# Optimization experiments

Hardware: AMD Instinct MI355X
Metric: run time of the kernel (lower is better)

## Reference

```python
import jax, jax.numpy as jnp
import numpy as np

IMAGE_TOKEN_INDEX = -200
B, N, D = 2, 768, 2048          # batch, seq, llm_size
CLIP = 1024                      # clip hidden size
NUM_HEADS = 8
HEAD_DIM = CLIP // NUM_HEADS
NUM_LAYER, LAYER_RATE = 24, 4
LAYER_IDX = np.asarray(NUM_LAYER - np.arange(0, NUM_LAYER + 1, LAYER_RATE))  # [24,20,16,12,8,4,0]
J = len(LAYER_IDX)               # 7 selected layers
L = NUM_LAYER + 1                # 25 stacked layers in all_features
IMG, PATCH = 336, 14
HP = IMG // PATCH                # 24 patches per side; patch_ratio == 1
HW = HP * HP                     # 576 vision tokens
SL = HP * (HP + 1) + 1           # 601 = H*(W+1)+1 ragged slice length
SCALE = CLIP ** (-0.5)
LN_EPS = 1e-5
COS_EPS = 1e-8


def setup_inputs() -> dict:
    key = jax.random.key(0)
    ks = jax.random.split(key, 10)
    input_ids = jax.random.randint(ks[0], (B, N), 0, 32000)
    pos = jnp.array([37, 111])  # image-token positions; pos + SL <= N
    input_ids = input_ids.at[jnp.arange(B), pos].set(IMAGE_TOKEN_INDEX)
    rgb = jax.random.normal(ks[1], (B, 3, IMG, IMG), dtype=jnp.float32)
    mask = jnp.ones((B, 1, IMG, IMG), dtype=jnp.float32)  # last channel: all-ones mask
    images = jnp.concatenate([rgb, mask], axis=1)
    all_features = jax.random.normal(ks[2], (B, N, L, D), dtype=jnp.float32)
    patch_hw = jnp.full((B, 2), HP, dtype=jnp.int32)
    s = 0.02
    return {
        'input_ids': input_ids,
        'images': images,
        'all_features': all_features,
        'patch_hw': patch_hw,
        'norm_gamma': jnp.ones((J, D), dtype=jnp.float32),
        'norm_beta': jnp.zeros((J, D), dtype=jnp.float32),
        'norm_w': jax.random.normal(ks[3], (J, CLIP, D), dtype=jnp.float32) * s,
        'input_w': jax.random.normal(ks[4], (CLIP, D), dtype=jnp.float32) * s,
        'input_b': jnp.zeros((CLIP,), dtype=jnp.float32),
        'output_w': jax.random.normal(ks[5], (CLIP, CLIP), dtype=jnp.float32) * s,
        'output_b': jnp.zeros((CLIP,), dtype=jnp.float32),
        'clip_w': jax.random.normal(ks[6], (CLIP, 3 * PATCH * PATCH), dtype=jnp.float32) * s,
        'clip_b': jnp.zeros((CLIP,), dtype=jnp.float32),
    }


def reference(input_ids, images, all_features, patch_hw,
              norm_gamma, norm_beta, norm_w,
              input_w, input_b, output_w, output_b, clip_w, clip_b):
    # clip_layer modeled as a frozen 14x14 patch-embed linear -> [B, HW, CLIP]
    patches = images[:, :3].reshape(B, 3, HP, PATCH, HP, PATCH)
    patches = patches.transpose(0, 2, 4, 1, 3, 5).reshape(B, HW, 3 * PATCH * PATCH)
    clip_feats = patches @ clip_w.T + clip_b  # [B, HW, CLIP]
    # mask channel is all ones -> pooled clip_2d_mask keeps every patch
    lidx = jnp.asarray(LAYER_IDX)

    def per_sample(ids, feats, cf):
        # ragged slice at the image token (data-dependent start, fixed length)
        idx = jnp.argmax(ids == IMAGE_TOKEN_INDEX)
        f = jax.lax.dynamic_slice_in_dim(feats, idx, SL, axis=0)[1:]      # [600, L, D]
        # [L,D,H,W+1] drop-last-col in torch == row-major split here
        f = f.reshape(HP, HP + 1, L, D)[:, :HP].reshape(HW, L, D)          # [576, L, D]
        # per-layer LayerNorm + no-bias Linear on 7 selected layers
        xj = f[:, lidx]                                                    # [HW, J, D]
        mu = xj.mean(-1, keepdims=True)
        var = ((xj - mu) ** 2).mean(-1, keepdims=True)
        xn = (xj - mu) / jnp.sqrt(var + LN_EPS) * norm_gamma + norm_beta
        vis = jnp.einsum('njd,jcd->njc', xn, norm_w)                       # [HW, J, CLIP]
        inp = f[:, -1] @ input_w.T + input_b                               # [HW, CLIP]
        # single-query multi-head cross attention over the J-1 kv layers
        q = vis[:, 0].reshape(HW, NUM_HEADS, HEAD_DIM)                     # [HW, h, d]
        kv = vis[:, 1:].reshape(HW, J - 1, NUM_HEADS, HEAD_DIM).transpose(0, 2, 1, 3)  # [HW, h, J-1, d]
        attn = jax.nn.softmax((q[:, :, None, :] * SCALE * kv).sum(-1), axis=-1)        # [HW, h, J-1]
        fuse = (attn[..., None] * kv).sum(-2).reshape(HW, CLIP)
        out = inp + fuse @ output_w.T + output_b                           # [HW, CLIP]
        denom = jnp.maximum(jnp.linalg.norm(out, axis=-1) * jnp.linalg.norm(cf, axis=-1), COS_EPS)
        cos = (out * cf).sum(-1) / denom
        return 1.0 - cos.mean()

    losses = jax.vmap(per_sample)(input_ids, all_features, clip_feats)
    return losses.mean()  # mse_loss / count_image with count_image == B
```

## Files before the change

kernel.cpp:

```cpp
#include <hip/hip_runtime.h>

#define HW_   576
#define BHW   1152
#define DD    2048
#define CLIPC 1024
#define NSEQ  768
#define LL    25
#define KPAD  640

#define ASCALE 8.0f
#define BSCALE 32.0f
#define INV_AB (1.0f/256.0f)

typedef __bf16 bf16x8 __attribute__((ext_vector_type(8)));
typedef float  f32x4  __attribute__((ext_vector_type(4)));
typedef int    i32x8  __attribute__((ext_vector_type(8)));
typedef unsigned short u16;
typedef unsigned char  u8;

__device__ __forceinline__ float bf2f(u16 u){
  union { unsigned int i; float f; } v; v.i = ((unsigned int)u) << 16; return v.f;
}
__device__ __forceinline__ u16 f2bf(float f){
  union { float f; unsigned int i; } v; v.f = f;
  unsigned int u = v.i;
  return (u16)((u + 0x7fffu + ((u >> 16) & 1u)) >> 16);
}
__device__ __forceinline__ unsigned int pk2bf(float a, float b){
  return ((unsigned int)f2bf(a)) | (((unsigned int)f2bf(b)) << 16);
}
__device__ __forceinline__ unsigned int pk4_fp8(float a, float b, float c, float d){
  int v = 0;
  v = __builtin_amdgcn_cvt_pk_fp8_f32(a, b, v, false);
  v = __builtin_amdgcn_cvt_pk_fp8_f32(c, d, v, true);
  return (unsigned int)v;
}

__device__ __forceinline__ void gld_lds16(const void* g, void* l){
  __builtin_amdgcn_global_load_lds((__attribute__((address_space(1))) void*)g,
                                   (__attribute__((address_space(3))) void*)l,
                                   16, 0, 0);
}

__global__ void setup_k(const int* __restrict__ ids, int* __restrict__ idxbuf,
                        float* __restrict__ rowacc){
  const int lane = threadIdx.x;
  for (int b = 0; b < 2; b++){
    int best = 0x7fffffff;
    for (int i = lane; i < NSEQ; i += 64)
      if (ids[b*NSEQ + i] == -200 && i < best) best = i;
    for (int off = 32; off; off >>= 1){ int o = __shfl_xor(best, off); best = min(best, o); }
    if (lane == 0) idxbuf[b] = best;
  }
  for (int i = lane; i < BHW*4; i += 64) rowacc[i] = 0.f;
}

__global__ void prep_k(const float* __restrict__ norm_w, const float* __restrict__ input_w,
                       const float* __restrict__ output_w, const float* __restrict__ clip_w,
                       const float* __restrict__ images, const float* __restrict__ feats,
                       const int* __restrict__ idxbuf,
                       const float* __restrict__ gamma, const float* __restrict__ beta,
                       u8* __restrict__ B8, u16* __restrict__ inpw, u16* __restrict__ outw,
                       u16* __restrict__ clipw, u16* __restrict__ patch,
                       u8* __restrict__ A8, u16* __restrict__ A7){
  const int blk = blockIdx.x, tid = threadIdx.x;
  if (blk < 7168){
    long idx = (long)blk*2048 + tid*8;
    float4 v0 = *(const float4*)(norm_w + idx);
    float4 v1 = *(const float4*)(norm_w + idx + 4);
    uint2 o;
    o.x = pk4_fp8(v0.x*BSCALE, v0.y*BSCALE, v0.z*BSCALE, v0.w*BSCALE);
    o.y = pk4_fp8(v1.x*BSCALE, v1.y*BSCALE, v1.z*BSCALE, v1.w*BSCALE);
    *(uint2*)(B8 + idx) = o;
    return;
  }
  if (blk < 8704){
    const bool isInp = (blk < 8192);
    long idx = (long)(blk - (isInp ? 7168 : 8192))*2048 + tid*8;
    const float* s = isInp ? (input_w + idx) : (output_w + idx);
    float4 v0 = *(const float4*)s;
    float4 v1 = *(const float4*)(s + 4);
    uint4 o = { pk2bf(v0.x,v0.y), pk2bf(v0.z,v0.w), pk2bf(v1.x,v1.y), pk2bf(v1.z,v1.w) };
    *(uint4*)((isInp ? inpw : outw) + idx) = o;
    return;
  }
  if (blk < 9728){
    const int c = blk - 8704;
    for (int k = tid; k < KPAD; k += 256)
      clipw[c*KPAD + k] = (k < 588) ? f2bf(clip_w[c*588 + k]) : (u16)0;
    return;
  }
  if (blk < 10880){
    const int r = blk - 9728;
    const int b = r / HW_, n = r % HW_;
    const int hi = n / 24, wi = n % 24;
    for (int p = tid; p < KPAD; p += 256){
      float v = 0.f;
      if (p < 588){
        int c3 = p / 196, rem = p - c3*196;
        int ph = rem / 14, pw = rem - ph*14;
        v = images[(((long)b*4 + c3)*336 + hi*14 + ph)*336 + wi*14 + pw];
      }
      patch[(long)r*KPAD + p] = f2bf(v);
    }
    return;
  }
  const int q = blk - 10880;
  const int r = q >> 3, g = q & 7;
  const int b = r / HW_, n = r % HW_;
  const int hi = n / 24, wi = n % 24;
  const int tok = idxbuf[b] + 1 + hi*25 + wi;
  const int layer = (g < 7) ? (24 - g*4) : 24;
  const float* src = feats + (((long)(b*NSEQ + tok))*LL + layer)*DD + tid*8;
  float4 a = *(const float4*)src;
  float4 c = *(const float4*)(src + 4);
  if (g == 7){
    uint4 o = { pk2bf(a.x,a.y), pk2bf(a.z,a.w), pk2bf(c.x,c.y), pk2bf(c.z,c.w) };
    *(uint4*)(A7 + (long)r*DD + tid*8) = o;
    return;
  }
  float s  = a.x+a.y+a.z+a.w + c.x+c.y+c.z+c.w;
  float qq = a.x*a.x+a.y*a.y+a.z*a.z+a.w*a.w + c.x*c.x+c.y*c.y+c.z*c.z+c.w*c.w;
  for (int off = 32; off; off >>= 1){ s += __shfl_xor(s, off); qq += __shfl_xor(qq, off); }
  __shared__ float rs[4], rq[4];
  const int wave = tid >> 6, lane = tid & 63;
  if (lane == 0){ rs[wave] = s; rq[wave] = qq; }
  __syncthreads();
  const float ts = rs[0]+rs[1]+rs[2]+rs[3];
  const float tq = rq[0]+rq[1]+rq[2]+rq[3];
  const float mu   = ts * (1.f/2048.f);
  const float var  = tq * (1.f/2048.f) - mu*mu;
  const float rstd = rsqrtf(var + 1e-5f);
  const float4 g0 = *(const float4*)(gamma + g*DD + tid*8);
  const float4 g1 = *(const float4*)(gamma + g*DD + tid*8 + 4);
  const float4 b0 = *(const float4*)(beta  + g*DD + tid*8);
  const float4 b1 = *(const float4*)(beta  + g*DD + tid*8 + 4);
  uint2 o;
  o.x = pk4_fp8(((a.x-mu)*rstd*g0.x + b0.x)*ASCALE, ((a.y-mu)*rstd*g0.y + b0.y)*ASCALE,
                ((a.z-mu)*rstd*g0.z + b0.z)*ASCALE, ((a.w-mu)*rstd*g0.w + b0.w)*ASCALE);
  o.y = pk4_fp8(((c.x-mu)*rstd*g1.x + b1.x)*ASCALE, ((c.y-mu)*rstd*g1.y + b1.y)*ASCALE,
                ((c.z-mu)*rstd*g1.z + b1.z)*ASCALE, ((c.w-mu)*rstd*g1.w + b1.w)*ASCALE);
  *(uint2*)(A8 + ((long)g*BHW + r)*DD + tid*8) = o;
}

__global__ __launch_bounds__(256, 3)
void gemm_fp8_k(const u8* __restrict__ A_all, const u8* __restrict__ B_all,
                u16* __restrict__ C_all){
  __shared__ alignas(16) u8 As[128*128];
  __shared__ alignas(16) u8 Bs[128*128];
  const int z = blockIdx.z;
  const u8* Az = A_all + (long)z*BHW*DD;
  const u8* Bz = B_all + (long)z*CLIPC*DD;
  const int bm = blockIdx.x*128, bn = blockIdx.y*128;
  const int tid = threadIdx.x, wave = tid >> 6, lane = tid & 63;
  const int l15 = lane & 15, quad = lane >> 4;
  const int wr = (wave >> 1)*64, wc = (wave & 1)*64;
  f32x4 acc[4][4] = {};

  const int laneRow   = lane >> 3;
  const int laneChunk = (lane & 7) ^ laneRow;
  const u8* gA = Az + (long)(bm + wave*32 + laneRow)*DD + laneChunk*16;
  const u8* gB = Bz + (long)(bn + wave*32 + laneRow)*DD + laneChunk*16;
  u8* lA = &As[wave*32*128];
  u8* lB = &Bs[wave*32*128];
  const long rs8 = 8L*DD;

  for (int k0 = 0; k0 < DD; k0 += 128){
#pragma unroll
    for (int t = 0; t < 4; t++) gld_lds16(gA + k0 + t*rs8, lA + t*1024);
#pragma unroll
    for (int t = 0; t < 4; t++) gld_lds16(gB + k0 + t*rs8, lB + t*1024);
    __syncthreads();
    i32x8 af[4], bg[4];
    const int sw = l15 & 7;
#pragma unroll
    for (int i = 0; i < 4; i++){
      const u8* rp = &As[(wr + i*16 + l15)*128];
      uint4 lo = *(const uint4*)(rp + (((quad*2 + 0) ^ sw)*16));
      uint4 hi = *(const uint4*)(rp + (((quad*2 + 1) ^ sw)*16));
      af[i] = (i32x8){(int)lo.x,(int)lo.y,(int)lo.z,(int)lo.w,
                      (int)hi.x,(int)hi.y,(int)hi.z,(int)hi.w};
    }
#pragma unroll
    for (int j = 0; j < 4; j++){
      const u8* rp = &Bs[(wc + j*16 + l15)*128];
      uint4 lo = *(const uint4*)(rp + (((quad*2 + 0) ^ sw)*16));
      uint4 hi = *(const uint4*)(rp + (((quad*2 + 1) ^ sw)*16));
      bg[j] = (i32x8){(int)lo.x,(int)lo.y,(int)lo.z,(int)lo.w,
                      (int)hi.x,(int)hi.y,(int)hi.z,(int)hi.w};
    }
#pragma unroll
    for (int i = 0; i < 4; i++)
#pragma unroll
      for (int j = 0; j < 4; j++)
        acc[i][j] = __builtin_amdgcn_mfma_scale_f32_16x16x128_f8f6f4(
            af[i], bg[j], acc[i][j], 0, 0, 0, 0x7F7F7F7F, 0, 0x7F7F7F7F);
    __syncthreads();
  }

  u16* C = C_all + (long)z*BHW*CLIPC;
#pragma unroll
  for (int i = 0; i < 4; i++)
#pragma unroll
    for (int j = 0; j < 4; j++)
#pragma unroll
      for (int rr = 0; rr < 4; rr++){
        const int row = bm + wr + i*16 + quad*4 + rr;
        const int col = bn + wc + j*16 + l15;
        C[(long)row*CLIPC + col] = f2bf(acc[i][j][rr] * INV_AB);
      }
}

__device__ __forceinline__ void gemm_core(const u16* __restrict__ Az, const u16* __restrict__ Bz,
                                          int K, int bm, int bn,
                                          u16* __restrict__ As, u16* __restrict__ Bs,
                                          f32x4 (&acc)[4][4]){
  const int tid  = threadIdx.x;
  const int wave = tid >> 6, lane = tid & 63;
  const int l15 = lane & 15, quad = lane >> 4;
  const int wr = (wave >> 1) * 64, wc = (wave & 1) * 64;
  const int laneRow = lane >> 3;
  const int laneCol = (((lane & 7) ^ laneRow) * 8);
  const u16* gA = Az + (long)(bm + wave*32 + laneRow)*K + laneCol;
  const u16* gB = Bz + (long)(bn + wave*32 + laneRow)*K + laneCol;
  u16* lA = &As[wave*2048];
  u16* lB = &Bs[wave*2048];
  const long rs8 = (long)8 * K;

  for (int k0 = 0; k0 < K; k0 += 64){
#pragma unroll
    for (int t = 0; t < 4; t++) gld_lds16(gA + k0 + t*rs8, lA + t*512);
#pragma unroll
    for (int t = 0; t < 4; t++) gld_lds16(gB + k0 + t*rs8, lB + t*512);
    __syncthreads();
#pragma unroll
    for (int s = 0; s < 2; s++){
      bf16x8 af[4], bg[4];
#pragma unroll
      for (int i = 0; i < 4; i++)
        af[i] = *(const bf16x8*)&As[(wr + i*16 + l15)*64 + (((s*4 + quad) ^ (l15 & 7)) * 8)];
#pragma unroll
      for (int j = 0; j < 4; j++)
        bg[j] = *(const bf16x8*)&Bs[(wc + j*16 + l15)*64 + (((s*4 + quad) ^ (l15 & 7)) * 8)];
#pragma unroll
      for (int i = 0; i < 4; i++)
#pragma unroll
        for (int j = 0; j < 4; j++)
          acc[i][j] = __builtin_amdgcn_mfma_f32_16x16x32_bf16(af[i], bg[j], acc[i][j], 0, 0, 0);
    }
    __syncthreads();
  }
}

__global__ __launch_bounds__(256, 3)
void gemm_misc_k(const u16* __restrict__ patch, const u16* __restrict__ clipw,
                 const u16* __restrict__ A7, const u16* __restrict__ inpw,
                 float* __restrict__ cf, u16* __restrict__ C7,
                 const float* __restrict__ clip_b, const float* __restrict__ input_b){
  __shared__ alignas(16) u16 As[128*64];
  __shared__ alignas(16) u16 Bs[128*64];
  const int z = blockIdx.z;
  const int bm = blockIdx.x*128, bn = blockIdx.y*128;
  const u16* Az = z ? A7 : patch;
  const u16* Bz = z ? inpw : clipw;
  const int K = z ? DD : KPAD;
  f32x4 acc[4][4] = {};
  gemm_core(Az, Bz, K, bm, bn, As, Bs, acc);

  const int lane = threadIdx.x & 63, wave = threadIdx.x >> 6;
  const int l15 = lane & 15, quad = lane >> 4;
  const int wr = (wave >> 1)*64, wc = (wave & 1)*64;
#pragma unroll
  for (int i = 0; i < 4; i++)
#pragma unroll
    for (int j = 0; j < 4; j++)
#pragma unroll
      for (int rr = 0; rr < 4; rr++){
        const int row = bm + wr + i*16 + quad*4 + rr;
        const int col = bn + wc + j*16 + l15;
        if (z) C7[(long)row*CLIPC + col] = f2bf(acc[i][j][rr] + input_b[col]);
        else   cf[(long)row*CLIPC + col] = acc[i][j][rr] + clip_b[col];
      }
}

__global__ void attn_k(const u16* __restrict__ C_all, u16* __restrict__ fuse){
  const int r = blockIdx.x;
  const int h = (blockIdx.y << 2) | (threadIdx.x >> 6);
  const int lane = threadIdx.x & 63;
  const long slot = (long)BHW * CLIPC;
  const long rb = (long)r * CLIPC;
  const int c0 = h*128 + lane, c1 = c0 + 64;
  const float q0 = bf2f(C_all[rb + c0]), q1 = bf2f(C_all[rb + c1]);
  float k0v[6], k1v[6], dt[6];
#pragma unroll
  for (int t = 0; t < 6; t++){
    const u16* base = C_all + (long)(t+1)*slot + rb;
    k0v[t] = bf2f(base[c0]); k1v[t] = bf2f(base[c1]);
    dt[t] = q0*k0v[t] + q1*k1v[t];
  }
#pragma unroll
  for (int t = 0; t < 6; t++)
    for (int off = 32; off; off >>= 1) dt[t] += __shfl_xor(dt[t], off);
  float l[6], e[6];
#pragma unroll
  for (int t = 0; t < 6; t++) l[t] = dt[t] * 0.03125f;
  float m = l[0];
#pragma unroll
  for (int t = 1; t < 6; t++) m = fmaxf(m, l[t]);
  float ssum = 0.f;
#pragma unroll
  for (int t = 0; t < 6; t++){ e[t] = __expf(l[t] - m); ssum += e[t]; }
  const float inv = 1.f / ssum;
  float f0 = 0.f, f1 = 0.f;
#pragma unroll
  for (int t = 0; t < 6; t++){ const float a = e[t]*inv; f0 += a*k0v[t]; f1 += a*k1v[t]; }
  fuse[rb + c0] = f2bf(f0);
  fuse[rb + c1] = f2bf(f1);
}

__global__ __launch_bounds__(256, 3)
void gemm_out_k(const u16* __restrict__ fuse, const u16* __restrict__ outw,
                const u16* __restrict__ inp, const float* __restrict__ output_b,
                const float* __restrict__ cf, float* __restrict__ rowacc){
  __shared__ alignas(16) u16 As[128*64];
  __shared__ alignas(16) u16 Bs[128*64];
  const int bm = blockIdx.x*128, bn = blockIdx.y*128;
  f32x4 acc[4][4] = {};
  gemm_core(fuse, outw, CLIPC, bm, bn, As, Bs, acc);

  const int lane = threadIdx.x & 63, wave = threadIdx.x >> 6;
  const int l15 = lane & 15, quad = lane >> 4;
  const int wr = (wave >> 1)*64, wc = (wave & 1)*64;
#pragma unroll
  for (int i = 0; i < 4; i++)
#pragma unroll
    for (int rr = 0; rr < 4; rr++){
      const int row = bm + wr + i*16 + quad*4 + rr;
      float soc = 0.f, soo = 0.f, scc = 0.f;
#pragma unroll
      for (int j = 0; j < 4; j++){
        const int col = bn + wc + j*16 + l15;
        const long p = (long)row*CLIPC + col;
        const float o = acc[i][j][rr] + output_b[col] + bf2f(inp[p]);
        const float c = cf[p];
        soc += o*c; soo += o*o; scc += c*c;
      }
#pragma unroll
      for (int off = 1; off < 16; off <<= 1){
        soc += __shfl_xor(soc, off); soo += __shfl_xor(soo, off); scc += __shfl_xor(scc, off);
      }
      if (l15 == 0){
        atomicAdd(&rowacc[row*4 + 0], soc);
        atomicAdd(&rowacc[row*4 + 1], soo);
        atomicAdd(&rowacc[row*4 + 2], scc);
      }
    }
}

__global__ void fin_k(const float* __restrict__ rowacc, float* __restrict__ out){
  const int tid = threadIdx.x;
  float s = 0.f;
  for (int r = tid; r < BHW; r += 256){
    const float soc = rowacc[r*4], soo = rowacc[r*4+1], scc = rowacc[r*4+2];
    s += soc / fmaxf(sqrtf(soo*scc), 1e-8f);
  }
  for (int off = 32; off; off >>= 1) s += __shfl_xor(s, off);
  __shared__ float rs[4];
  const int wave = tid >> 6, lane = tid & 63;
  if (lane == 0) rs[wave] = s;
  __syncthreads();
  if (tid == 0) out[0] = 1.f - (rs[0]+rs[1]+rs[2]+rs[3]) * (1.f/(float)BHW);
}

extern "C" void kernel_launch(void* const* d_in, const int* in_sizes, int n_in,
                              void* d_out, int out_size, void* d_ws, size_t ws_size,
                              hipStream_t stream){
  const int*   input_ids = (const int*)  d_in[0];
  const float* images    = (const float*)d_in[1];
  const float* all_feats = (const float*)d_in[2];
  const float* norm_gamma = (const float*)d_in[4];
  const float* norm_beta  = (const float*)d_in[5];
  const float* norm_w     = (const float*)d_in[6];
  const float* input_w    = (const float*)d_in[7];
  const float* input_b    = (const float*)d_in[8];
  const float* output_w   = (const float*)d_in[9];
  const float* output_b   = (const float*)d_in[10];
  const float* clip_w     = (const float*)d_in[11];
  const float* clip_b     = (const float*)d_in[12];
  float* out = (float*)d_out;

  char* w = (char*)d_ws;
  int*   idxbuf = (int*)w;
  size_t off = 256;
  u8*  A8    = (u8*) (w + off); off += 7L*BHW*DD;
  u16* A7    = (u16*)(w + off); off += (long)BHW*DD*2;
  u8*  B8    = (u8*) (w + off); off += 7L*CLIPC*DD;
  u16* inpw  = (u16*)(w + off); off += (long)CLIPC*DD*2;
  u16* outw  = (u16*)(w + off); off += (long)CLIPC*CLIPC*2;
  u16* clipw = (u16*)(w + off); off += (long)CLIPC*KPAD*2;
  u16* patch = (u16*)(w + off); off += (long)BHW*KPAD*2;
  u16* C_all = (u16*)(w + off); off += 8L*BHW*CLIPC*2;
  u16* fuse  = (u16*)(w + off); off += (long)BHW*CLIPC*2;
  float* cf     = (float*)(w + off); off += (long)BHW*CLIPC*4;
  float* rowacc = (float*)(w + off); off += (long)BHW*4*4;

  setup_k<<<1, 64, 0, stream>>>(input_ids, idxbuf, rowacc);
  prep_k<<<20096, 256, 0, stream>>>(norm_w, input_w, output_w, clip_w, images, all_feats,
                                    idxbuf, norm_gamma, norm_beta,
                                    B8, inpw, outw, clipw, patch, A8, A7);
  gemm_fp8_k<<<dim3(9, 8, 7), 256, 0, stream>>>(A8, B8, C_all);
  gemm_misc_k<<<dim3(9, 8, 2), 256, 0, stream>>>(patch, clipw, A7, inpw, cf,
                                                 C_all + 7L*BHW*CLIPC, clip_b, input_b);
  attn_k<<<dim3(1152, 2), 256, 0, stream>>>(C_all, fuse);
  gemm_out_k<<<dim3(9, 8), 256, 0, stream>>>(fuse, outw, C_all + 7L*BHW*CLIPC,
                                             output_b, cf, rowacc);
  fin_k<<<1, 256, 0, stream>>>(rowacc, out);
}
```

Baseline: 554.7 us.

## Fold setup and finalize kernels into neighbors and merge GEMM launches

Removes the single-block setup kernel by having each feature-gather block scan input_ids for the image token itself, and zeroes rowacc inside prep_k. Merges the fp8 and bf16 misc GEMMs into one launch with nine z-slices. Replaces the finalize kernel with a last-block-done atomic counter in gemm_out_k. This cuts three launches and their serialization gaps, at the cost of redundant id scans in many blocks and a grid-wide atomic handshake.

```diff
diff --git a/kernel.cpp b/kernel.cpp
--- a/kernel.cpp
+++ b/kernel.cpp
@@ -42,27 +42,15 @@
                                    16, 0, 0);
 }
 
-__global__ void setup_k(const int* __restrict__ ids, int* __restrict__ idxbuf,
-                        float* __restrict__ rowacc){
-  const int lane = threadIdx.x;
-  for (int b = 0; b < 2; b++){
-    int best = 0x7fffffff;
-    for (int i = lane; i < NSEQ; i += 64)
-      if (ids[b*NSEQ + i] == -200 && i < best) best = i;
-    for (int off = 32; off; off >>= 1){ int o = __shfl_xor(best, off); best = min(best, o); }
-    if (lane == 0) idxbuf[b] = best;
-  }
-  for (int i = lane; i < BHW*4; i += 64) rowacc[i] = 0.f;
-}
-
 __global__ void prep_k(const float* __restrict__ norm_w, const float* __restrict__ input_w,
                        const float* __restrict__ output_w, const float* __restrict__ clip_w,
                        const float* __restrict__ images, const float* __restrict__ feats,
-                       const int* __restrict__ idxbuf,
+                       const int* __restrict__ ids,
                        const float* __restrict__ gamma, const float* __restrict__ beta,
                        u8* __restrict__ B8, u16* __restrict__ inpw, u16* __restrict__ outw,
                        u16* __restrict__ clipw, u16* __restrict__ patch,
-                       u8* __restrict__ A8, u16* __restrict__ A7){
+                       u8* __restrict__ A8, u16* __restrict__ A7,
+                       float* __restrict__ rowacc, unsigned int* __restrict__ done){
   const int blk = blockIdx.x, tid = threadIdx.x;
   if (blk < 7168){
     long idx = (long)blk*2048 + tid*8;
@@ -88,6 +76,10 @@
     const int c = blk - 8704;
     for (int k = tid; k < KPAD; k += 256)
       clipw[c*KPAD + k] = (k < 588) ? f2bf(clip_w[c*588 + k]) : (u16)0;
+    if (blk == 8704){
+      for (int i = tid; i < BHW*4; i += 256) rowacc[i] = 0.f;
+      if (tid == 0) *done = 0u;
+    }
     return;
   }
   if (blk < 10880){
@@ -109,7 +101,17 @@
   const int r = q >> 3, g = q & 7;
   const int b = r / HW_, n = r % HW_;
   const int hi = n / 24, wi = n % 24;
-  const int tok = idxbuf[b] + 1 + hi*25 + wi;
+  __shared__ int ridx[4];
+  __shared__ float rs[4], rq[4];
+  {
+    int best = 0x7fffffff;
+    for (int i = tid; i < NSEQ; i += 256)
+      if (ids[b*NSEQ + i] == -200 && i < best) best = i;
+    for (int off = 32; off; off >>= 1){ int o = __shfl_xor(best, off); best = min(best, o); }
+    if ((tid & 63) == 0) ridx[tid >> 6] = best;
+    __syncthreads();
+  }
+  const int tok = min(min(ridx[0],ridx[1]),min(ridx[2],ridx[3])) + 1 + hi*25 + wi;
   const int layer = (g < 7) ? (24 - g*4) : 24;
   const float* src = feats + (((long)(b*NSEQ + tok))*LL + layer)*DD + tid*8;
   float4 a = *(const float4*)src;
@@ -122,7 +124,6 @@
   float s  = a.x+a.y+a.z+a.w + c.x+c.y+c.z+c.w;
   float qq = a.x*a.x+a.y*a.y+a.z*a.z+a.w*a.w + c.x*c.x+c.y*c.y+c.z*c.z+c.w*c.w;
   for (int off = 32; off; off >>= 1){ s += __shfl_xor(s, off); qq += __shfl_xor(qq, off); }
-  __shared__ float rs[4], rq[4];
   const int wave = tid >> 6, lane = tid & 63;
   if (lane == 0){ rs[wave] = s; rq[wave] = qq; }
   __syncthreads();
@@ -144,143 +145,134 @@
 }
 
 __global__ __launch_bounds__(256, 3)
-void gemm_fp8_k(const u8* __restrict__ A_all, const u8* __restrict__ B_all,
-                u16* __restrict__ C_all){
-  __shared__ alignas(16) u8 As[128*128];
-  __shared__ alignas(16) u8 Bs[128*128];
+void gemm9_k(const u8* __restrict__ A8, const u8* __restrict__ B8,
+             u16* __restrict__ C_all, const u16* __restrict__ A7,
+             const u16* __restrict__ inpw, const u16* __restrict__ patch,
+             const u16* __restrict__ clipw, float* __restrict__ cf,
+             const float* __restrict__ input_b, const float* __restrict__ clip_b){
+  __shared__ alignas(16) u8 smem[32768];
   const int z = blockIdx.z;
-  const u8* Az = A_all + (long)z*BHW*DD;
-  const u8* Bz = B_all + (long)z*CLIPC*DD;
   const int bm = blockIdx.x*128, bn = blockIdx.y*128;
   const int tid = threadIdx.x, wave = tid >> 6, lane = tid & 63;
   const int l15 = lane & 15, quad = lane >> 4;
   const int wr = (wave >> 1)*64, wc = (wave & 1)*64;
   f32x4 acc[4][4] = {};
-
   const int laneRow   = lane >> 3;
   const int laneChunk = (lane & 7) ^ laneRow;
-  const u8* gA = Az + (long)(bm + wave*32 + laneRow)*DD + laneChunk*16;
-  const u8* gB = Bz + (long)(bn + wave*32 + laneRow)*DD + laneChunk*16;
-  u8* lA = &As[wave*32*128];
-  u8* lB = &Bs[wave*32*128];
-  const long rs8 = 8L*DD;
-
-  for (int k0 = 0; k0 < DD; k0 += 128){
-#pragma unroll
-    for (int t = 0; t < 4; t++) gld_lds16(gA + k0 + t*rs8, lA + t*1024);
-#pragma unroll
-    for (int t = 0; t < 4; t++) gld_lds16(gB + k0 + t*rs8, lB + t*1024);
-    __syncthreads();
-    i32x8 af[4], bg[4];
-    const int sw = l15 & 7;
-#pragma unroll
-    for (int i = 0; i < 4; i++){
-      const u8* rp = &As[(wr + i*16 + l15)*128];
-      uint4 lo = *(const uint4*)(rp + (((quad*2 + 0) ^ sw)*16));
-      uint4 hi = *(const uint4*)(rp + (((quad*2 + 1) ^ sw)*16));
-      af[i] = (i32x8){(int)lo.x,(int)lo.y,(int)lo.z,(int)lo.w,
-                      (int)hi.x,(int)hi.y,(int)hi.z,(int)hi.w};
-    }
-#pragma unroll
-    for (int j = 0; j < 4; j++){
-      const u8* rp = &Bs[(wc + j*16 + l15)*128];
-      uint4 lo = *(const uint4*)(rp + (((quad*2 + 0) ^ sw)*16));
-      uint4 hi = *(const uint4*)(rp + (((quad*2 + 1) ^ sw)*16));
-      bg[j] = (i32x8){(int)lo.x,(int)lo.y,(int)lo.z,(int)lo.w,
-                      (int)hi.x,(int)hi.y,(int)hi.z,(int)hi.w};
-    }
+
+  if (z < 7){
+    u8* As = smem;
+    u8* Bs = smem + 16384;
+    const u8* Az = A8 + (long)z*BHW*DD;
+    const u8* Bz = B8 + (long)z*CLIPC*DD;
+    const u8* gA = Az + (long)(bm + wave*32 + laneRow)*DD + laneChunk*16;
+    const u8* gB = Bz + (long)(bn + wave*32 + laneRow)*DD + laneChunk*16;
+    u8* lA = &As[wave*32*128];
+    u8* lB = &Bs[wave*32*128];
+    const long rs8 = 8L*DD;
+    for (int k0 = 0; k0 < DD; k0 += 128){
+#pragma unroll
+      for (int t = 0; t < 4; t++) gld_lds16(gA + k0 + t*rs8, lA + t*1024);
+#pragma unroll
+      for (int t = 0; t < 4; t++) gld_lds16(gB + k0 + t*rs8, lB + t*1024);
+      __syncthreads();
+      i32x8 af[4], bg[4];
+      const int sw = l15 & 7;
+#pragma unroll
+      for (int i = 0; i < 4; i++){
+        const u8* rp = &As[(wr + i*16 + l15)*128];
+        uint4 lo = *(const uint4*)(rp + (((quad*2 + 0) ^ sw)*16));
+        uint4 hi = *(const uint4*)(rp + (((quad*2 + 1) ^ sw)*16));
+        af[i] = (i32x8){(int)lo.x,(int)lo.y,(int)lo.z,(int)lo.w,
+                        (int)hi.x,(int)hi.y,(int)hi.z,(int)hi.w};
+      }
+#pragma unroll
+      for (int j = 0; j < 4; j++){
+        const u8* rp = &Bs[(wc + j*16 + l15)*128];
+        uint4 lo = *(const uint4*)(rp + (((quad*2 + 0) ^ sw)*16));
+        uint4 hi = *(const uint4*)(rp + (((quad*2 + 1) ^ sw)*16));
+        bg[j] = (i32x8){(int)lo.x,(int)lo.y,(int)lo.z,(int)lo.w,
+                        (int)hi.x,(int)hi.y,(int)hi.z,(int)hi.w};
+      }
+#pragma unroll
+      for (int i = 0; i < 4; i++)
+#pragma unroll
+        for (int j = 0; j < 4; j++)
+          acc[i][j] = __builtin_amdgcn_mfma_scale_f32_16x16x128_f8f6f4(
+              af[i], bg[j], acc[i][j], 0, 0, 0, 0x7F7F7F7F, 0, 0x7F7F7F7F);
+      __syncthreads();
+    }
+    u16* C = C_all + (long)z*BHW*CLIPC;
 #pragma unroll
     for (int i = 0; i < 4; i++)
 #pragma unroll
       for (int j = 0; j < 4; j++)
-        acc[i][j] = __builtin_amdgcn_mfma_scale_f32_16x16x128_f8f6f4(
-            af[i], bg[j], acc[i][j], 0, 0, 0, 0x7F7F7F7F, 0, 0x7F7F7F7F);
-    __syncthreads();
-  }
-
-  u16* C = C_all + (long)z*BHW*CLIPC;
-#pragma unroll
-  for (int i = 0; i < 4; i++)
-#pragma unroll
-    for (int j = 0; j < 4; j++)
-#pragma unroll
-      for (int rr = 0; rr < 4; rr++){
-        const int row = bm + wr + i*16 + quad*4 + rr;
-        const int col = bn + wc + j*16 + l15;
-        C[(long)row*CLIPC + col] = f2bf(acc[i][j][rr] * INV_AB);
-      }
-}
-
-__device__ __forceinline__ void gemm_core(const u16* __restrict__ Az, const u16* __restrict__ Bz,
-                                          int K, int bm, int bn,
-                                          u16* __restrict__ As, u16* __restrict__ Bs,
-                                          f32x4 (&acc)[4][4]){
-  const int tid  = threadIdx.x;
-  const int wave = tid >> 6, lane = tid & 63;
-  const int l15 = lane & 15, quad = lane >> 4;
-  const int wr = (wave >> 1) * 64, wc = (wave & 1) * 64;
-  const int laneRow = lane >> 3;
-  const int laneCol = (((lane & 7) ^ laneRow) * 8);
-  const u16* gA = Az + (long)(bm + wave*32 + laneRow)*K + laneCol;
-  const u16* gB = Bz + (long)(bn + wave*32 + laneRow)*K + laneCol;
-  u16* lA = &As[wave*2048];
-  u16* lB = &Bs[wave*2048];
-  const long rs8 = (long)8 * K;
-
-  for (int k0 = 0; k0 < K; k0 += 64){
-#pragma unroll
-    for (int t = 0; t < 4; t++) gld_lds16(gA + k0 + t*rs8, lA + t*512);
-#pragma unroll
-    for (int t = 0; t < 4; t++) gld_lds16(gB + k0 + t*rs8, lB + t*512);
-    __syncthreads();
-#pragma unroll
-    for (int s = 0; s < 2; s++){
-      bf16x8 af[4], bg[4];
+#pragma unroll
+        for (int rr = 0; rr < 4; rr++){
+          const int row = bm + wr + i*16 + quad*4 + rr;
+          const int col = bn + wc + j*16 + l15;
+          C[(long)row*CLIPC + col] = f2bf(acc[i][j][rr] * INV_AB);
+        }
+  } else {
+    u16* As = (u16*)smem;
+    u16* Bs = (u16*)(smem + 16384);
+    const u16* Az = (z == 7) ? A7   : patch;
+    const u16* Bz = (z == 7) ? inpw : clipw;
+    const int K  = (z == 7) ? DD : KPAD;
+    const int laneCol = laneChunk * 8;
+    const u16* gA = Az + (long)(bm + wave*32 + laneRow)*K + laneCol;
+    const u16* gB = Bz + (long)(bn + wave*32 + laneRow)*K + laneCol;
+    u16* lA = &As[wave*2048];
+    u16* lB = &Bs[wave*2048];
+    const long rs8 = (long)8 * K;
+    for (int k0 = 0; k0 < K; k0 += 64){
+#pragma unroll
+      for (int t = 0; t < 4; t++) gld_lds16(gA + k0 + t*rs8, lA + t*512);
+#pragma unroll
+      for (int t = 0; t < 4; t++) gld_lds16(gB + k0 + t*rs8, lB + t*512);
+      __syncthreads();
+#pragma unroll
+      for (int s = 0; s < 2; s++){
+        bf16x8 af[4], bg[4];
+#pragma unroll
+        for (int i = 0; i < 4; i++)
+          af[i] = *(const bf16x8*)&As[(wr + i*16 + l15)*64 + (((s*4 + quad) ^ (l15 & 7))*8)];
+#pragma unroll
+        for (int j = 0; j < 4; j++)
+          bg[j] = *(const bf16x8*)&Bs[(wc + j*16 + l15)*64 + (((s*4 + quad) ^ (l15 & 7))*8)];
+#pragma unroll
+        for (int i = 0; i < 4; i++)
+#pragma unroll
+          for (int j = 0; j < 4; j++)
+            acc[i][j] = __builtin_amdgcn_mfma_f32_16x16x32_bf16(af[i], bg[j], acc[i][j], 0, 0, 0);
+      }
+      __syncthreads();
+    }
+    if (z == 7){
+      u16* C = C_all + 7L*BHW*CLIPC;
 #pragma unroll
       for (int i = 0; i < 4; i++)
-        af[i] = *(const bf16x8*)&As[(wr + i*16 + l15)*64 + (((s*4 + quad) ^ (l15 & 7)) * 8)];
-#pragma unroll
-      for (int j = 0; j < 4; j++)
-        bg[j] = *(const bf16x8*)&Bs[(wc + j*16 + l15)*64 + (((s*4 + quad) ^ (l15 & 7)) * 8)];
+#pragma unroll
+        for (int j = 0; j < 4; j++)
+#pragma unroll
+          for (int rr = 0; rr < 4; rr++){
+            const int row = bm + wr + i*16 + quad*4 + rr;
+            const int col = bn + wc + j*16 + l15;
+            C[(long)row*CLIPC + col] = f2bf(acc[i][j][rr] + input_b[col]);
+          }
+    } else {
 #pragma unroll
       for (int i = 0; i < 4; i++)
 #pragma unroll
         for (int j = 0; j < 4; j++)
-          acc[i][j] = __builtin_amdgcn_mfma_f32_16x16x32_bf16(af[i], bg[j], acc[i][j], 0, 0, 0);
-    }
-    __syncthreads();
-  }
-}
-
-__global__ __launch_bounds__(256, 3)
-void gemm_misc_k(const u16* __restrict__ patch, const u16* __restrict__ clipw,
-                 const u16* __restrict__ A7, const u16* __restrict__ inpw,
-                 float* __restrict__ cf, u16* __restrict__ C7,
-                 const float* __restrict__ clip_b, const float* __restrict__ input_b){
-  __shared__ alignas(16) u16 As[128*64];
-  __shared__ alignas(16) u16 Bs[128*64];
-  const int z = blockIdx.z;
-  const int bm = blockIdx.x*128, bn = blockIdx.y*128;
-  const u16* Az = z ? A7 : patch;
-  const u16* Bz = z ? inpw : clipw;
-  const int K = z ? DD : KPAD;
-  f32x4 acc[4][4] = {};
-  gemm_core(Az, Bz, K, bm, bn, As, Bs, acc);
-
-  const int lane = threadIdx.x & 63, wave = threadIdx.x >> 6;
-  const int l15 = lane & 15, quad = lane >> 4;
-  const int wr = (wave >> 1)*64, wc = (wave & 1)*64;
-#pragma unroll
-  for (int i = 0; i < 4; i++)
-#pragma unroll
-    for (int j = 0; j < 4; j++)
-#pragma unroll
-      for (int rr = 0; rr < 4; rr++){
-        const int row = bm + wr + i*16 + quad*4 + rr;
-        const int col = bn + wc + j*16 + l15;
-        if (z) C7[(long)row*CLIPC + col] = f2bf(acc[i][j][rr] + input_b[col]);
-        else   cf[(long)row*CLIPC + col] = acc[i][j][rr] + clip_b[col];
-      }
+#pragma unroll
+          for (int rr = 0; rr < 4; rr++){
+            const int row = bm + wr + i*16 + quad*4 + rr;
+            const int col = bn + wc + j*16 + l15;
+            cf[(long)row*CLIPC + col] = acc[i][j][rr] + clip_b[col];
+          }
+    }
+  }
 }
 
 __global__ void attn_k(const u16* __restrict__ C_all, u16* __restrict__ fuse){
@@ -321,16 +313,48 @@
 __global__ __launch_bounds__(256, 3)
 void gemm_out_k(const u16* __restrict__ fuse, const u16* __restrict__ outw,
                 const u16* __restrict__ inp, const float* __restrict__ output_b,
-                const float* __restrict__ cf, float* __restrict__ rowacc){
-  __shared__ alignas(16) u16 As[128*64];
-  __shared__ alignas(16) u16 Bs[128*64];
+                const float* __restrict__ cf, float* __restrict__ rowacc,
+                unsigned int* __restrict__ done, float* __restrict__ out){
+  __shared__ alignas(16) u8 smem[32768];
+  u16* As = (u16*)smem;
+  u16* Bs = (u16*)(smem + 16384);
   const int bm = blockIdx.x*128, bn = blockIdx.y*128;
-  f32x4 acc[4][4] = {};
-  gemm_core(fuse, outw, CLIPC, bm, bn, As, Bs, acc);
-
-  const int lane = threadIdx.x & 63, wave = threadIdx.x >> 6;
+  const int tid = threadIdx.x, wave = tid >> 6, lane = tid & 63;
   const int l15 = lane & 15, quad = lane >> 4;
   const int wr = (wave >> 1)*64, wc = (wave & 1)*64;
+  f32x4 acc[4][4] = {};
+  {
+    const int laneRow = lane >> 3;
+    const int laneCol = (((lane & 7) ^ laneRow) * 8);
+    const u16* gA = fuse + (long)(bm + wave*32 + laneRow)*CLIPC + laneCol;
+    const u16* gB = outw + (long)(bn + wave*32 + laneRow)*CLIPC + laneCol;
+    u16* lA = &As[wave*2048];
+    u16* lB = &Bs[wave*2048];
+    const long rs8 = 8L*CLIPC;
+    for (int k0 = 0; k0 < CLIPC; k0 += 64){
+#pragma unroll
+      for (int t = 0; t < 4; t++) gld_lds16(gA + k0 + t*rs8, lA + t*512);
+#pragma unroll
+      for (int t = 0; t < 4; t++) gld_lds16(gB + k0 + t*rs8, lB + t*512);
+      __syncthreads();
+#pragma unroll
+      for (int s = 0; s < 2; s++){
+        bf16x8 af[4], bg[4];
+#pragma unroll
+        for (int i = 0; i < 4; i++)
+          af[i] = *(const bf16x8*)&As[(wr + i*16 + l15)*64 + (((s*4 + quad) ^ (l15 & 7))*8)];
+#pragma unroll
+        for (int j = 0; j < 4; j++)
+          bg[j] = *(const bf16x8*)&Bs[(wc + j*16 + l15)*64 + (((s*4 + quad) ^ (l15 & 7))*8)];
+#pragma unroll
+        for (int i = 0; i < 4; i++)
+#pragma unroll
+          for (int j = 0; j < 4; j++)
+            acc[i][j] = __builtin_amdgcn_mfma_f32_16x16x32_bf16(af[i], bg[j], acc[i][j], 0, 0, 0);
+      }
+      __syncthreads();
+    }
+  }
 #pragma unroll
   for (int i = 0; i < 4; i++)
 #pragma unroll
@@ -355,21 +379,23 @@
         atomicAdd(&rowacc[row*4 + 2], scc);
       }
     }
-}
-
-__global__ void fin_k(const float* __restrict__ rowacc, float* __restrict__ out){
-  const int tid = threadIdx.x;
+  __threadfence();
+  __shared__ unsigned int amLast;
+  if (tid == 0) amLast = (atomicAdd(done, 1u) == 71u) ? 1u : 0u;
+  __syncthreads();
+  if (!amLast) return;
   float s = 0.f;
   for (int r = tid; r < BHW; r += 256){
-    const float soc = rowacc[r*4], soo = rowacc[r*4+1], scc = rowacc[r*4+2];
+    const float soc = __hip_atomic_load(&rowacc[r*4+0], __ATOMIC_RELAXED, __HIP_MEMORY_SCOPE_AGENT);
+    const float soo = __hip_atomic_load(&rowacc[r*4+1], __ATOMIC_RELAXED, __HIP_MEMORY_SCOPE_AGENT);
+    const float scc = __hip_atomic_load(&rowacc[r*4+2], __ATOMIC_RELAXED, __HIP_MEMORY_SCOPE_AGENT);
     s += soc / fmaxf(sqrtf(soo*scc), 1e-8f);
   }
   for (int off = 32; off; off >>= 1) s += __shfl_xor(s, off);
-  __shared__ float rs[4];
-  const int wave = tid >> 6, lane = tid & 63;
-  if (lane == 0) rs[wave] = s;
+  __shared__ float fr[4];
+  if ((tid & 63) == 0) fr[tid >> 6] = s;
   __syncthreads();
-  if (tid == 0) out[0] = 1.f - (rs[0]+rs[1]+rs[2]+rs[3]) * (1.f/(float)BHW);
+  if (tid == 0) out[0] = 1.f - (fr[0]+fr[1]+fr[2]+fr[3]) * (1.f/(float)BHW);
 }
 
 extern "C" void kernel_launch(void* const* d_in, const int* in_sizes, int n_in,
@@ -390,7 +416,7 @@
   float* out = (float*)d_out;
 
   char* w = (char*)d_ws;
-  int*   idxbuf = (int*)w;
+  unsigned int* done = (unsigned int*)w;
   size_t off = 256;
   u8*  A8    = (u8*) (w + off); off += 7L*BHW*DD;
   u16* A7    = (u16*)(w + off); off += (long)BHW*DD*2;
@@ -404,15 +430,12 @@
   float* cf     = (float*)(w + off); off += (long)BHW*CLIPC*4;
   float* rowacc = (float*)(w + off); off += (long)BHW*4*4;
 
-  setup_k<<<1, 64, 0, stream>>>(input_ids, idxbuf, rowacc);
   prep_k<<<20096, 256, 0, stream>>>(norm_w, input_w, output_w, clip_w, images, all_feats,
-                                    idxbuf, norm_gamma, norm_beta,
-                                    B8, inpw, outw, clipw, patch, A8, A7);
-  gemm_fp8_k<<<dim3(9, 8, 7), 256, 0, stream>>>(A8, B8, C_all);
-  gemm_misc_k<<<dim3(9, 8, 2), 256, 0, stream>>>(patch, clipw, A7, inpw, cf,
-                                                 C_all + 7L*BHW*CLIPC, clip_b, input_b);
+                                    input_ids, norm_gamma, norm_beta,
+                                    B8, inpw, outw, clipw, patch, A8, A7, rowacc, done);
+  gemm9_k<<<dim3(9, 8, 9), 256, 0, stream>>>(A8, B8, C_all, A7, inpw, patch, clipw, cf,
+                                             input_b, clip_b);
   attn_k<<<dim3(1152, 2), 256, 0, stream>>>(C_all, fuse);
   gemm_out_k<<<dim3(9, 8), 256, 0, stream>>>(fuse, outw, C_all + 7L*BHW*CLIPC,
-                                             output_b, cf, rowacc);
-  fin_k<<<1, 256, 0, stream>>>(rowacc, out);
-}
+                                             output_b, cf, rowacc, done, out);
+}
```

Measured after the change: 531.9 us. -4.1%, faster.
